# Optimization experiments

Measured on AMD Instinct MI355X. Metric: run time of the kernel, lower is better.

The kernel has to match this reference:

```python
import jax, jax.numpy as jnp
import numpy as np

NUM_HEADS = 16
ROPE_THETA = 10000.0


def setup_inputs() -> dict:
    key = jax.random.key(0)
    k1, k2, k3 = jax.random.split(key, 3)
    B, T, C = 2, 2048, 1024
    x = jax.random.normal(k1, (B, T, C), dtype=jnp.float32)
    w_qkv = jax.random.normal(k2, (3 * C, C), dtype=jnp.float32) * 0.02
    w_out = jax.random.normal(k3, (C, C), dtype=jnp.float32) * 0.02
    return {"x": x, "w_qkv": w_qkv, "w_out": w_out}


def _apply_rope(x, cos, sin):
    # x: (B, H, T, D); interleaved complex pairs: (x[...,2i], x[...,2i+1])
    B, H, T, D = x.shape
    xp = x.reshape(B, H, T, D // 2, 2)
    xr, xi = xp[..., 0], xp[..., 1]
    # cos/sin: (T, D//2) broadcast over (B, H)
    out_r = xr * cos - xi * sin
    out_i = xr * sin + xi * cos
    return jnp.stack([out_r, out_i], axis=-1).reshape(B, H, T, D)


def reference(x, w_qkv, w_out):
    B, T, C = x.shape
    H = NUM_HEADS
    D = C // H
    scale = 1.0 / np.sqrt(D).astype(np.float32)

    qkv = x @ w_qkv.T                      # (B, T, 3C)
    q, k, v = jnp.split(qkv, 3, axis=-1)

    def to_heads(t):
        return t.reshape(B, T, H, D).transpose(0, 2, 1, 3)  # (B, H, T, D)

    q, k, v = to_heads(q), to_heads(k), to_heads(v)

    # RoPE frequencies: freqs[t, j] = t / theta^(2j/D)
    inv_freq = 1.0 / (ROPE_THETA ** (jnp.arange(0, D, 2, dtype=jnp.float32) / D))
    freqs = jnp.arange(T, dtype=jnp.float32)[:, None] * inv_freq[None, :]  # (T, D//2)
    cos, sin = jnp.cos(freqs), jnp.sin(freqs)

    q = _apply_rope(q, cos, sin)
    k = _apply_rope(k, cos, sin)

    att = jnp.einsum('bhqd,bhkd->bhqk', q, k) * scale   # (B, H, T, T)
    causal = jnp.tril(jnp.ones((T, T), dtype=bool))
    att = jnp.where(causal[None, None], att, -jnp.inf)
    att = jax.nn.softmax(att, axis=-1)
    # dropout p=0.0 (eval) -> identity

    out = jnp.einsum('bhqk,bhkd->bhqd', att, v)          # (B, H, T, D)
    out = out.transpose(0, 2, 1, 3).reshape(B, T, C)
    return out @ w_out.T
```

## Files before the change

kernel.cpp:

```cpp
#include <hip/hip_runtime.h>
#include <hip/hip_bf16.h>
#include <math.h>

#define DEV __device__ __forceinline__

typedef float  floatx4 __attribute__((ext_vector_type(4)));
typedef short  bf16x8  __attribute__((ext_vector_type(8)));

typedef __attribute__((address_space(1))) void gvoid;
typedef __attribute__((address_space(3))) void lvoid;

static constexpr int Bc = 2, Tc = 2048, Cc = 1024, Hc = 16, Dc = 64;

DEV void gload16(const void* g, void* l) {
    __builtin_amdgcn_global_load_lds((gvoid*)g, (lvoid*)l, 16, 0, 0);
}

__global__ void prep_kernel(const float* __restrict__ xf,
                            const float* __restrict__ wqkvf,
                            const float* __restrict__ woutf,
                            __hip_bfloat16* __restrict__ xb,
                            __hip_bfloat16* __restrict__ wqkvb,
                            __hip_bfloat16* __restrict__ woutb,
                            float* __restrict__ cosT, float* __restrict__ sinT) {
    int gb = blockIdx.x;
    if (gb < 8192) {
        const float* src; __hip_bfloat16* dst; int i;
        if (gb < 4096)      { src = xf;    dst = xb;    i = gb * 256 + threadIdx.x; }
        else if (gb < 7168) { src = wqkvf; dst = wqkvb; i = (gb - 4096) * 256 + threadIdx.x; }
        else                { src = woutf; dst = woutb; i = (gb - 7168) * 256 + threadIdx.x; }
        float4 f = ((const float4*)src)[i];
        union { ushort4 u; __hip_bfloat16 h[4]; } pk;
        pk.h[0] = __float2bfloat16(f.x);
        pk.h[1] = __float2bfloat16(f.y);
        pk.h[2] = __float2bfloat16(f.z);
        pk.h[3] = __float2bfloat16(f.w);
        ((ushort4*)dst)[i] = pk.u;
    } else {
        int i = (gb - 8192) * 256 + threadIdx.x;
        int t = i >> 5, j = i & 31;
        float invf = powf(10000.0f, -(float)j / 32.0f);
        float f = (float)t * invf;
        cosT[i] = cosf(f);
        sinT[i] = sinf(f);
    }
}

template <int EPI>
__global__ __launch_bounds__(256, 2) void gemm_bt(
    const __hip_bfloat16* __restrict__ A,
    const __hip_bfloat16* __restrict__ Bm,
    float* __restrict__ Cout,
    __hip_bfloat16* __restrict__ qb,
    __hip_bfloat16* __restrict__ kb,
    __hip_bfloat16* __restrict__ vb,
    const float* __restrict__ cosT,
    const float* __restrict__ sinT,
    int K)
{
    __shared__ __align__(16) __hip_bfloat16 SM[2 * 128 * 64];
    __hip_bfloat16* const As = SM;
    __hip_bfloat16* const Bs = SM + 128 * 64;

    const int tid  = threadIdx.x;
    const int lane = tid & 63, wave = tid >> 6;
    const int quad = lane >> 4, cidx = lane & 15;
    const int wm = wave & 1, wn = wave >> 1;
    const int bm = blockIdx.x * 128, bn = blockIdx.y * 128;

    floatx4 acc[4][4] = {};

    for (int k0 = 0; k0 < K; k0 += 64) {
#pragma unroll
        for (int it = 0; it < 4; ++it) {
            int idx = tid + it * 256;
            int r = idx >> 3, cs = idx & 7;
            int cg = cs ^ (r & 7);
            gload16(A  + (size_t)(bm + r) * K + k0 + cg * 8, As + idx * 8);
            gload16(Bm + (size_t)(bn + r) * K + k0 + cg * 8, Bs + idx * 8);
        }
        __syncthreads();
#pragma unroll
        for (int ks = 0; ks < 2; ++ks) {
            bf16x8 af[4], bf[4];
#pragma unroll
            for (int mt = 0; mt < 4; ++mt) {
                int r = wm * 64 + mt * 16 + cidx;
                af[mt] = *(const bf16x8*)(As + (r * 8 + ((ks * 4 + quad) ^ (r & 7))) * 8);
            }
#pragma unroll
            for (int nt = 0; nt < 4; ++nt) {
                int r = wn * 64 + nt * 16 + cidx;
                bf[nt] = *(const bf16x8*)(Bs + (r * 8 + ((ks * 4 + quad) ^ (r & 7))) * 8);
            }
#pragma unroll
            for (int mt = 0; mt < 4; ++mt)
#pragma unroll
                for (int nt = 0; nt < 4; ++nt)
                    acc[mt][nt] = __builtin_amdgcn_mfma_f32_16x16x32_bf16(
                        af[mt], bf[nt], acc[mt][nt], 0, 0, 0);
        }
        __syncthreads();
    }

    if constexpr (EPI == 0) {
#pragma unroll
        for (int mt = 0; mt < 4; ++mt)
#pragma unroll
            for (int nt = 0; nt < 4; ++nt) {
                int n = bn + wn * 64 + nt * 16 + cidx;
#pragma unroll
                for (int reg = 0; reg < 4; ++reg) {
                    int m = bm + wm * 64 + mt * 16 + quad * 4 + reg;
                    Cout[(size_t)m * 1024 + n] = acc[mt][nt][reg];
                }
            }
    } else if (bn >= 2048) {
#pragma unroll
        for (int nt = 0; nt < 4; ++nt) {
            int n_l = wn * 64 + nt * 16 + cidx;
#pragma unroll
            for (int mt = 0; mt < 4; ++mt)
#pragma unroll
                for (int reg = 0; reg < 4; ++reg) {
                    int m_l = wm * 64 + mt * 16 + quad * 4 + reg;
                    SM[n_l * 128 + (((m_l >> 3) ^ (n_l & 15)) * 8) + (m_l & 7)] =
                        __float2bfloat16(acc[mt][nt][reg]);
                }
        }
        __syncthreads();
        {
            int b = bm >> 11, t0 = bm & 2047;
            int c = tid & 15;
#pragma unroll
            for (int it = 0; it < 8; ++it) {
                int row = it * 16 + (tid >> 4);
                int cc = (bn - 2048) + row;
                int h = cc >> 6, d = cc & 63;
                *(uint4*)(vb + ((size_t)(b * Hc + h) * Dc + d) * Tc + t0 + c * 8) =
                    *(const uint4*)(SM + row * 128 + ((c ^ (row & 15)) * 8));
            }
        }
    } else {
        const float SL2E = 0.125f * 1.44269504088896f;
#pragma unroll
        for (int nt = 0; nt < 4; ++nt) {
            int n   = bn + wn * 64 + nt * 16 + cidx;
            int sec = n >> 10;
            int cc  = n & 1023;
            int h = cc >> 6, d = cc & 63, j = d >> 1;
            __hip_bfloat16* dst = (sec == 0) ? qb : kb;
#pragma unroll
            for (int mt = 0; mt < 4; ++mt) {
#pragma unroll
                for (int reg = 0; reg < 4; ++reg) {
                    int m = bm + wm * 64 + mt * 16 + quad * 4 + reg;
                    int b = m >> 11, t = m & 2047;
                    float v = acc[mt][nt][reg];
                    float p = __shfl_xor(v, 1);
                    float cz = cosT[t * 32 + j];
                    float sz = sinT[t * 32 + j];
                    float o = (d & 1) ? (p * sz + v * cz) : (v * cz - p * sz);
                    if (sec == 0) o *= SL2E;
                    dst[((size_t)(b * Hc + h) * Tc + t) * Dc + d] = __float2bfloat16(o);
                }
            }
        }
    }
}

__global__ __launch_bounds__(256, 2) void attn_kernel(
    const __hip_bfloat16* __restrict__ qb,
    const __hip_bfloat16* __restrict__ kb,
    const __hip_bfloat16* __restrict__ vb,
    __hip_bfloat16* __restrict__ ob)
{
    __shared__ __align__(16) __hip_bfloat16 Ks[128 * 64];
    __shared__ __align__(16) __hip_bfloat16 Vt[64 * 128];
    __shared__ __align__(16) __hip_bfloat16 Ps[4 * 64 * 32];
    __shared__ float Ls[4][64];

    const int tid  = threadIdx.x;
    const int lane = tid & 63, wave = tid >> 6;
    const int quad = lane >> 4, cidx = lane & 15;
    const int id = blockIdx.x;
    const int xcd = id & 7, s = id >> 3;
    const int bh = xcd * 4 + (s >> 4);
    const int bx = s & 15;
    const int b = bh >> 4, h = bh & 15;
    const size_t plane = (size_t)bh * Tc * Dc;
    const __hip_bfloat16* Vp = vb + plane;

    for (int half = 0; half < 2; ++half) {
        const int qt = half ? bx : 31 - bx;
        const int qbase = qt * 64;
        const int ktmax = (qbase + 63) >> 7;

#pragma unroll
        for (int it = 0; it < 2; ++it) {
            int idx = tid + it * 256;
            int r = idx >> 3, cs = idx & 7;
            int cg = cs ^ (r & 7);
            gload16(qb + plane + (size_t)(qbase + r) * 64 + cg * 8, Vt + idx * 8);
        }
#pragma unroll
        for (int it = 0; it < 4; ++it) {
            int idx = tid + it * 256;
            int r = idx >> 3, cs = idx & 7;
            int cg = cs ^ (r & 7);
            gload16(kb + plane + (size_t)r * 64 + cg * 8, Ks + idx * 8);
        }
        __syncthreads();
        bf16x8 qf[4][2];
#pragma unroll
        for (int mt = 0; mt < 4; ++mt)
#pragma unroll
            for (int ks = 0; ks < 2; ++ks) {
                int r = mt * 16 + cidx;
                qf[mt][ks] = *(const bf16x8*)(Vt + (r * 8 + ((ks * 4 + quad) ^ (r & 7))) * 8);
            }
        __syncthreads();

        floatx4 oacc[4][4] = {};
        float lsum[4][4] = {};
        __hip_bfloat16* const myP = Ps + wave * 2048;

        for (int kt = 0; kt <= ktmax; ++kt) {
#pragma unroll
            for (int it = 0; it < 4; ++it) {
                int idx = tid + it * 256;
                int r = idx >> 4, cs = idx & 15;
                int c = cs ^ (r & 15);
                gload16(Vp + (size_t)r * Tc + kt * 128 + c * 8, Vt + idx * 8);
            }

            floatx4 sacc[4][2] = {};
#pragma unroll
            for (int ks = 0; ks < 2; ++ks) {
                bf16x8 kf[2];
#pragma unroll
                for (int nt2 = 0; nt2 < 2; ++nt2) {
                    int r = wave * 32 + nt2 * 16 + cidx;
                    kf[nt2] = *(const bf16x8*)(Ks + (r * 8 + ((ks * 4 + quad) ^ (r & 7))) * 8);
                }
#pragma unroll
                for (int mt = 0; mt < 4; ++mt)
#pragma unroll
                    for (int nt2 = 0; nt2 < 2; ++nt2)
                        sacc[mt][nt2] = __builtin_amdgcn_mfma_f32_16x16x32_bf16(
                            qf[mt][ks], kf[nt2], sacc[mt][nt2], 0, 0, 0);
            }

            const bool domask = (kt == ktmax);
#pragma unroll
            for (int mt = 0; mt < 4; ++mt)
#pragma unroll
                for (int nt2 = 0; nt2 < 2; ++nt2) {
                    int n = kt * 128 + wave * 32 + nt2 * 16 + cidx;
                    int kl = nt2 * 16 + cidx;
#pragma unroll
                    for (int reg = 0; reg < 4; ++reg) {
                        int m = qbase + mt * 16 + quad * 4 + reg;
                        float p = __builtin_amdgcn_exp2f(sacc[mt][nt2][reg]);
                        if (domask && n > m) p = 0.0f;
                        lsum[mt][reg] += p;
                        int pr = reg * 16 + mt * 4 + quad;
                        int slot = (kl >> 3) ^ reg ^ ((quad >> 1) << 1);
                        myP[pr * 32 + slot * 8 + (kl & 7)] = __float2bfloat16(p);
                    }
                }

            __syncthreads();

            if (kt < ktmax) {
#pragma unroll
                for (int it = 0; it < 4; ++it) {
                    int idx = tid + it * 256;
                    int r = idx >> 3, cs = idx & 7;
                    int cg = cs ^ (r & 7);
                    gload16(kb + plane + (size_t)((kt + 1) * 128 + r) * 64 + cg * 8,
                            Ks + idx * 8);
                }
            }

            bf16x8 af[4];
#pragma unroll
            for (int mt = 0; mt < 4; ++mt) {
                int pr = (cidx & 3) * 16 + mt * 4 + (cidx >> 2);
                int slot = quad ^ (cidx & 3) ^ (((cidx >> 3) & 1) << 1);
                af[mt] = *(const bf16x8*)(myP + pr * 32 + slot * 8);
            }
#pragma unroll
            for (int dt = 0; dt < 4; ++dt) {
                int d = dt * 16 + cidx;
                bf16x8 vf = *(const bf16x8*)(Vt + (d * 16 + ((wave * 4 + quad) ^ (d & 15))) * 8);
#pragma unroll
                for (int mt = 0; mt < 4; ++mt)
                    oacc[mt][dt] = __builtin_amdgcn_mfma_f32_16x16x32_bf16(
                        af[mt], vf, oacc[mt][dt], 0, 0, 0);
            }
            __syncthreads();
        }

#pragma unroll
        for (int off = 1; off < 16; off <<= 1)
#pragma unroll
            for (int mt = 0; mt < 4; ++mt)
#pragma unroll
                for (int reg = 0; reg < 4; ++reg)
                    lsum[mt][reg] += __shfl_xor(lsum[mt][reg], off);
        if (cidx == 0)
#pragma unroll
            for (int mt = 0; mt < 4; ++mt)
#pragma unroll
                for (int reg = 0; reg < 4; ++reg)
                    Ls[wave][mt * 16 + quad * 4 + reg] = lsum[mt][reg];

        if (wave != 0) {
            float* dstw = (wave == 1) ? (float*)Ks : (wave == 2) ? (float*)Vt : (float*)Ps;
#pragma unroll
            for (int mt = 0; mt < 4; ++mt)
#pragma unroll
                for (int dt = 0; dt < 4; ++dt) {
                    int d = dt * 16 + cidx;
                    ((floatx4*)dstw)[d * 16 + ((mt * 4 + quad) ^ cidx)] = oacc[mt][dt];
                }
        }
        __syncthreads();
        if (wave == 0) {
#pragma unroll
            for (int mt = 0; mt < 4; ++mt)
#pragma unroll
                for (int dt = 0; dt < 4; ++dt) {
                    int d = dt * 16 + cidx;
                    int i = d * 16 + ((mt * 4 + quad) ^ cidx);
                    oacc[mt][dt] += ((const floatx4*)Ks)[i];
                    oacc[mt][dt] += ((const floatx4*)Vt)[i];
                    oacc[mt][dt] += ((const floatx4*)Ps)[i];
                }
#pragma unroll
            for (int mt = 0; mt < 4; ++mt)
#pragma unroll
                for (int reg = 0; reg < 4; ++reg) {
                    int q = mt * 16 + quad * 4 + reg;
                    float lt = Ls[0][q] + Ls[1][q] + Ls[2][q] + Ls[3][q];
                    float inv = 1.0f / lt;
#pragma unroll
                    for (int dt = 0; dt < 4; ++dt)
                        Ks[q * 64 + dt * 16 + cidx] =
                            __float2bfloat16(oacc[mt][dt][reg] * inv);
                }
        }
        __syncthreads();
#pragma unroll
        for (int i = 0; i < 2; ++i) {
            int c = tid * 2 + i;
            int row = c >> 3, col = c & 7;
            *(uint4*)(ob + (size_t)(b * Tc + qbase + row) * Cc + h * 64 + col * 8) =
                *(const uint4*)(Ks + row * 64 + col * 8);
        }
        __syncthreads();
    }
}

extern "C" void kernel_launch(void* const* d_in, const int* in_sizes, int n_in,
                              void* d_out, int out_size, void* d_ws, size_t ws_size,
                              hipStream_t stream) {
    const float* xf = nullptr; const float* wqkvf = nullptr; const float* woutf = nullptr;
    for (int i = 0; i < n_in; ++i) {
        if      (in_sizes[i] == 2 * 2048 * 1024) xf    = (const float*)d_in[i];
        else if (in_sizes[i] == 3 * 1024 * 1024) wqkvf = (const float*)d_in[i];
        else if (in_sizes[i] == 1024 * 1024)     woutf = (const float*)d_in[i];
    }
    float* out = (float*)d_out;

    char* ws = (char*)d_ws;
    const size_t MB = 1024 * 1024;
    __hip_bfloat16* qb    = (__hip_bfloat16*)(ws);
    __hip_bfloat16* kb    = (__hip_bfloat16*)(ws + 8  * MB);
    __hip_bfloat16* vb    = (__hip_bfloat16*)(ws + 16 * MB);
    __hip_bfloat16* ab    = (__hip_bfloat16*)(ws + 24 * MB);
    float* cosT           = (float*)(ws + 32 * MB);
    float* sinT           = (float*)(ws + 32 * MB + 256 * 1024);
    __hip_bfloat16* xb    = (__hip_bfloat16*)(ws + 33 * MB);
    __hip_bfloat16* wqkvb = (__hip_bfloat16*)(ws + 41 * MB);
    __hip_bfloat16* woutb = (__hip_bfloat16*)(ws + 47 * MB);

    prep_kernel<<<dim3(8448), dim3(256), 0, stream>>>(
        xf, wqkvf, woutf, xb, wqkvb, woutb, cosT, sinT);

    gemm_bt<1><<<dim3(32, 24), dim3(256), 0, stream>>>(
        xb, wqkvb, nullptr, qb, kb, vb, cosT, sinT, 1024);
    attn_kernel<<<dim3(512), dim3(256), 0, stream>>>(qb, kb, vb, ab);
    gemm_bt<0><<<dim3(32, 8), dim3(256), 0, stream>>>(
        ab, woutb, out, nullptr, nullptr, nullptr, nullptr, nullptr, 1024);
}
```

Baseline: 181.1 us.

## Keep P in registers via transposed QK^T and write attention output head-major

The attention kernel now computes S transposed (K as the A operand), so the probability tile lands in registers in the layout the 16x16x16 MFMA needs for the PV product. This removes the per-tile shared-memory round-trip for P. The attention output is stored per head (B,H,T,D) with a swizzled bf16x4 staging layout. A new dedicated output-projection GEMM uses 64x128 tiles (twice as many blocks) and gathers A rows straight from the head-major buffer. The trade-off is twice as many smaller MFMAs for PV, and a strided A gather in the final GEMM.

```diff
diff --git a/kernel.cpp b/kernel.cpp
--- a/kernel.cpp
+++ b/kernel.cpp
@@ -6,6 +6,7 @@
 
 typedef float  floatx4 __attribute__((ext_vector_type(4)));
 typedef short  bf16x8  __attribute__((ext_vector_type(8)));
+typedef short  bf16x4  __attribute__((ext_vector_type(4)));
 
 typedef __attribute__((address_space(1))) void gvoid;
 typedef __attribute__((address_space(3))) void lvoid;
@@ -46,11 +47,9 @@
     }
 }
 
-template <int EPI>
-__global__ __launch_bounds__(256, 2) void gemm_bt(
+__global__ __launch_bounds__(256, 2) void gemm_qkv(
     const __hip_bfloat16* __restrict__ A,
     const __hip_bfloat16* __restrict__ Bm,
-    float* __restrict__ Cout,
     __hip_bfloat16* __restrict__ qb,
     __hip_bfloat16* __restrict__ kb,
     __hip_bfloat16* __restrict__ vb,
@@ -103,19 +102,7 @@
         __syncthreads();
     }
 
-    if constexpr (EPI == 0) {
-#pragma unroll
-        for (int mt = 0; mt < 4; ++mt)
-#pragma unroll
-            for (int nt = 0; nt < 4; ++nt) {
-                int n = bn + wn * 64 + nt * 16 + cidx;
-#pragma unroll
-                for (int reg = 0; reg < 4; ++reg) {
-                    int m = bm + wm * 64 + mt * 16 + quad * 4 + reg;
-                    Cout[(size_t)m * 1024 + n] = acc[mt][nt][reg];
-                }
-            }
-    } else if (bn >= 2048) {
+    if (bn >= 2048) {
 #pragma unroll
         for (int nt = 0; nt < 4; ++nt) {
             int n_l = wn * 64 + nt * 16 + cidx;
@@ -169,6 +156,78 @@
     }
 }
 
+__global__ __launch_bounds__(256, 2) void gemm_out(
+    const __hip_bfloat16* __restrict__ A,
+    const __hip_bfloat16* __restrict__ Bm,
+    float* __restrict__ Cout)
+{
+    __shared__ __align__(16) __hip_bfloat16 As[64 * 64];
+    __shared__ __align__(16) __hip_bfloat16 Bs[128 * 64];
+
+    const int tid  = threadIdx.x;
+    const int lane = tid & 63, wave = tid >> 6;
+    const int quad = lane >> 4, cidx = lane & 15;
+    const int bm = blockIdx.x * 64, bn = blockIdx.y * 128;
+    const int K = 1024;
+
+    floatx4 acc[4][2] = {};
+
+    for (int k0 = 0; k0 < K; k0 += 64) {
+        int h = k0 >> 6;
+#pragma unroll
+        for (int it = 0; it < 2; ++it) {
+            int idx = tid + it * 256;
+            int r = idx >> 3, cs = idx & 7;
+            int cg = cs ^ (r & 7);
+            int m = bm + r;
+            const __hip_bfloat16* src =
+                A + ((size_t)((m >> 11) * 16 + h) * 2048 + (m & 2047)) * 64 + cg * 8;
+            gload16(src, As + idx * 8);
+        }
+#pragma unroll
+        for (int it = 0; it < 4; ++it) {
+            int idx = tid + it * 256;
+            int r = idx >> 3, cs = idx & 7;
+            int cg = cs ^ (r & 7);
+            gload16(Bm + (size_t)(bn + r) * K + k0 + cg * 8, Bs + idx * 8);
+        }
+        __syncthreads();
+#pragma unroll
+        for (int ks = 0; ks < 2; ++ks) {
+            bf16x8 af[4], bf[2];
+#pragma unroll
+            for (int mt = 0; mt < 4; ++mt) {
+                int r = mt * 16 + cidx;
+                af[mt] = *(const bf16x8*)(As + (r * 8 + ((ks * 4 + quad) ^ (r & 7))) * 8);
+            }
+#pragma unroll
+            for (int nt = 0; nt < 2; ++nt) {
+                int r = wave * 32 + nt * 16 + cidx;
+                bf[nt] = *(const bf16x8*)(Bs + (r * 8 + ((ks * 4 + quad) ^ (r & 7))) * 8);
+            }
+#pragma unroll
+            for (int mt = 0; mt < 4; ++mt)
+#pragma unroll
+                for (int nt = 0; nt < 2; ++nt)
+                    acc[mt][nt] = __builtin_amdgcn_mfma_f32_16x16x32_bf16(
+                        af[mt], bf[nt], acc[mt][nt], 0, 0, 0);
+        }
+        __syncthreads();
+    }
+
+#pragma unroll
+    for (int mt = 0; mt < 4; ++mt)
+#pragma unroll
+        for (int nt = 0; nt < 2; ++nt) {
+            int n = bn + wave * 32 + nt * 16 + cidx;
+#pragma unroll
+            for (int reg = 0; reg < 4; ++reg) {
+                int m = bm + mt * 16 + quad * 4 + reg;
+                Cout[(size_t)m * 1024 + n] = acc[mt][nt][reg];
+            }
+        }
+}
+
 __global__ __launch_bounds__(256, 2) void attn_kernel(
     const __hip_bfloat16* __restrict__ qb,
     const __hip_bfloat16* __restrict__ kb,
@@ -177,7 +236,7 @@
 {
     __shared__ __align__(16) __hip_bfloat16 Ks[128 * 64];
     __shared__ __align__(16) __hip_bfloat16 Vt[64 * 128];
-    __shared__ __align__(16) __hip_bfloat16 Ps[4 * 64 * 32];
+    __shared__ __align__(16) __hip_bfloat16 Ps[128 * 64];
     __shared__ float Ls[4][64];
 
     const int tid  = threadIdx.x;
@@ -187,7 +246,6 @@
     const int xcd = id & 7, s = id >> 3;
     const int bh = xcd * 4 + (s >> 4);
     const int bx = s & 15;
-    const int b = bh >> 4, h = bh & 15;
     const size_t plane = (size_t)bh * Tc * Dc;
     const __hip_bfloat16* Vp = vb + plane;
 
@@ -221,9 +279,8 @@
             }
         __syncthreads();
 
-        floatx4 oacc[4][4] = {};
-        float lsum[4][4] = {};
-        __hip_bfloat16* const myP = Ps + wave * 2048;
+        floatx4 oaccT[4][4] = {};
+        float lsum[4] = {0.f, 0.f, 0.f, 0.f};
 
         for (int kt = 0; kt <= ktmax; ++kt) {
 #pragma unroll
@@ -248,27 +305,27 @@
 #pragma unroll
                     for (int nt2 = 0; nt2 < 2; ++nt2)
                         sacc[mt][nt2] = __builtin_amdgcn_mfma_f32_16x16x32_bf16(
-                            qf[mt][ks], kf[nt2], sacc[mt][nt2], 0, 0, 0);
+                            kf[nt2], qf[mt][ks], sacc[mt][nt2], 0, 0, 0);
             }
 
             const bool domask = (kt == ktmax);
-#pragma unroll
-            for (int mt = 0; mt < 4; ++mt)
+            bf16x4 pf[4][2];
+#pragma unroll
+            for (int mt = 0; mt < 4; ++mt) {
+                int q = qbase + mt * 16 + cidx;
 #pragma unroll
                 for (int nt2 = 0; nt2 < 2; ++nt2) {
-                    int n = kt * 128 + wave * 32 + nt2 * 16 + cidx;
-                    int kl = nt2 * 16 + cidx;
 #pragma unroll
                     for (int reg = 0; reg < 4; ++reg) {
-                        int m = qbase + mt * 16 + quad * 4 + reg;
+                        int key = kt * 128 + wave * 32 + nt2 * 16 + quad * 4 + reg;
                         float p = __builtin_amdgcn_exp2f(sacc[mt][nt2][reg]);
-                        if (domask && n > m) p = 0.0f;
-                        lsum[mt][reg] += p;
-                        int pr = reg * 16 + mt * 4 + quad;
-                        int slot = (kl >> 3) ^ reg ^ ((quad >> 1) << 1);
-                        myP[pr * 32 + slot * 8 + (kl & 7)] = __float2bfloat16(p);
+                        if (domask && key > q) p = 0.0f;
+                        lsum[mt] += p;
+                        __hip_bfloat16 hb = __float2bfloat16(p);
+                        pf[mt][nt2][reg] = *(const short*)&hb;
                     }
                 }
+            }
 
             __syncthreads();
 
@@ -283,81 +340,77 @@
                 }
             }
 
-            bf16x8 af[4];
-#pragma unroll
-            for (int mt = 0; mt < 4; ++mt) {
-                int pr = (cidx & 3) * 16 + mt * 4 + (cidx >> 2);
-                int slot = quad ^ (cidx & 3) ^ (((cidx >> 3) & 1) << 1);
-                af[mt] = *(const bf16x8*)(myP + pr * 32 + slot * 8);
-            }
 #pragma unroll
             for (int dt = 0; dt < 4; ++dt) {
                 int d = dt * 16 + cidx;
-                bf16x8 vf = *(const bf16x8*)(Vt + (d * 16 + ((wave * 4 + quad) ^ (d & 15))) * 8);
-#pragma unroll
-                for (int mt = 0; mt < 4; ++mt)
-                    oacc[mt][dt] = __builtin_amdgcn_mfma_f32_16x16x32_bf16(
-                        af[mt], vf, oacc[mt][dt], 0, 0, 0);
+#pragma unroll
+                for (int ks2 = 0; ks2 < 2; ++ks2) {
+                    int chunk = wave * 4 + ks2 * 2 + (quad >> 1);
+                    bf16x4 vtf = *(const bf16x4*)(
+                        Vt + (d * 16 + (chunk ^ (d & 15))) * 8 + (quad & 1) * 4);
+#pragma unroll
+                    for (int mt = 0; mt < 4; ++mt)
+                        oaccT[mt][dt] = __builtin_amdgcn_mfma_f32_16x16x16bf16_1k(
+                            vtf, pf[mt][ks2], oaccT[mt][dt], 0, 0, 0);
+                }
             }
             __syncthreads();
         }
 
 #pragma unroll
-        for (int off = 1; off < 16; off <<= 1)
-#pragma unroll
-            for (int mt = 0; mt < 4; ++mt)
-#pragma unroll
-                for (int reg = 0; reg < 4; ++reg)
-                    lsum[mt][reg] += __shfl_xor(lsum[mt][reg], off);
-        if (cidx == 0)
-#pragma unroll
-            for (int mt = 0; mt < 4; ++mt)
-#pragma unroll
-                for (int reg = 0; reg < 4; ++reg)
-                    Ls[wave][mt * 16 + quad * 4 + reg] = lsum[mt][reg];
+        for (int off = 16; off < 64; off <<= 1)
+#pragma unroll
+            for (int mt = 0; mt < 4; ++mt)
+                lsum[mt] += __shfl_xor(lsum[mt], off);
+        if (quad == 0)
+#pragma unroll
+            for (int mt = 0; mt < 4; ++mt)
+                Ls[wave][mt * 16 + cidx] = lsum[mt];
 
         if (wave != 0) {
             float* dstw = (wave == 1) ? (float*)Ks : (wave == 2) ? (float*)Vt : (float*)Ps;
 #pragma unroll
             for (int mt = 0; mt < 4; ++mt)
 #pragma unroll
+                for (int dt = 0; dt < 4; ++dt)
+                    ((floatx4*)dstw)[(mt * 4 + dt) * 64 + lane] = oaccT[mt][dt];
+        }
+        __syncthreads();
+        if (wave == 0) {
+#pragma unroll
+            for (int mt = 0; mt < 4; ++mt)
+#pragma unroll
                 for (int dt = 0; dt < 4; ++dt) {
-                    int d = dt * 16 + cidx;
-                    ((floatx4*)dstw)[d * 16 + ((mt * 4 + quad) ^ cidx)] = oacc[mt][dt];
-                }
-        }
-        __syncthreads();
-        if (wave == 0) {
-#pragma unroll
-            for (int mt = 0; mt < 4; ++mt)
+                    int i = (mt * 4 + dt) * 64 + lane;
+                    oaccT[mt][dt] += ((const floatx4*)Ks)[i];
+                    oaccT[mt][dt] += ((const floatx4*)Vt)[i];
+                    oaccT[mt][dt] += ((const floatx4*)Ps)[i];
+                }
+#pragma unroll
+            for (int mt = 0; mt < 4; ++mt) {
+                int q = mt * 16 + cidx;
+                float lt = Ls[0][q] + Ls[1][q] + Ls[2][q] + Ls[3][q];
+                float inv = 1.0f / lt;
 #pragma unroll
                 for (int dt = 0; dt < 4; ++dt) {
-                    int d = dt * 16 + cidx;
-                    int i = d * 16 + ((mt * 4 + quad) ^ cidx);
-                    oacc[mt][dt] += ((const floatx4*)Ks)[i];
-                    oacc[mt][dt] += ((const floatx4*)Vt)[i];
-                    oacc[mt][dt] += ((const floatx4*)Ps)[i];
-                }
-#pragma unroll
-            for (int mt = 0; mt < 4; ++mt)
-#pragma unroll
-                for (int reg = 0; reg < 4; ++reg) {
-                    int q = mt * 16 + quad * 4 + reg;
-                    float lt = Ls[0][q] + Ls[1][q] + Ls[2][q] + Ls[3][q];
-                    float inv = 1.0f / lt;
-#pragma unroll
-                    for (int dt = 0; dt < 4; ++dt)
-                        Ks[q * 64 + dt * 16 + cidx] =
-                            __float2bfloat16(oacc[mt][dt][reg] * inv);
-                }
+                    bf16x4 o4;
+#pragma unroll
+                    for (int reg = 0; reg < 4; ++reg) {
+                        __hip_bfloat16 hb = __float2bfloat16(oaccT[mt][dt][reg] * inv);
+                        o4[reg] = *(const short*)&hb;
+                    }
+                    int g = dt * 4 + quad;
+                    *(bf16x4*)(Ks + q * 64 + (g ^ (q & 12)) * 4) = o4;
+                }
+            }
         }
         __syncthreads();
 #pragma unroll
         for (int i = 0; i < 2; ++i) {
             int c = tid * 2 + i;
-            int row = c >> 3, col = c & 7;
-            *(uint4*)(ob + (size_t)(b * Tc + qbase + row) * Cc + h * 64 + col * 8) =
-                *(const uint4*)(Ks + row * 64 + col * 8);
+            int row = c >> 3, cp = c & 7;
+            *(uint4*)(ob + plane + (size_t)(qbase + row) * 64 + cp * 8) =
+                *(const uint4*)(Ks + row * 64 + ((cp * 2) ^ (row & 12)) * 4);
         }
         __syncthreads();
     }
@@ -389,9 +442,8 @@
     prep_kernel<<<dim3(8448), dim3(256), 0, stream>>>(
         xf, wqkvf, woutf, xb, wqkvb, woutb, cosT, sinT);
 
-    gemm_bt<1><<<dim3(32, 24), dim3(256), 0, stream>>>(
-        xb, wqkvb, nullptr, qb, kb, vb, cosT, sinT, 1024);
+    gemm_qkv<<<dim3(32, 24), dim3(256), 0, stream>>>(
+        xb, wqkvb, qb, kb, vb, cosT, sinT, 1024);
     attn_kernel<<<dim3(512), dim3(256), 0, stream>>>(qb, kb, vb, ab);
-    gemm_bt<0><<<dim3(32, 8), dim3(256), 0, stream>>>(
-        ab, woutb, out, nullptr, nullptr, nullptr, nullptr, nullptr, 1024);
-}
+    gemm_out<<<dim3(64, 8), dim3(256), 0, stream>>>(ab, woutb, out);
+}
```

After: 176.5 us. -2.5%, faster.
